# Kernel optimization log

Hardware: AMD Instinct MI355X
Metric: run time of the kernel (lower is better)

## Reference

```python
import jax, jax.numpy as jnp
import numpy as np

D_MODEL = 1024
N_HEADS = 16
HEAD_DIM = D_MODEL // N_HEADS
Q_PROJ = D_MODEL // 2
KV_PROJ = D_MODEL
INIT_SCALE = 0.02
EPS = 1e-5


def _ln(x, g, b):
    mu = jnp.mean(x, axis=-1, keepdims=True)
    var = jnp.mean(jnp.square(x - mu), axis=-1, keepdims=True)
    return (x - mu) * jax.lax.rsqrt(var + EPS) * g + b


def setup_inputs() -> dict:
    key = jax.random.key(0)
    ks = jax.random.split(key, 8)
    B, S = 2, 2048
    x = jax.random.normal(ks[0], (B, S, D_MODEL), dtype=jnp.float32)
    W_dq = INIT_SCALE * jax.random.normal(ks[1], (D_MODEL, Q_PROJ), dtype=jnp.float32)
    W_uq = INIT_SCALE * jax.random.normal(ks[2], (Q_PROJ, D_MODEL), dtype=jnp.float32)
    W_dkv = INIT_SCALE * jax.random.normal(ks[3], (D_MODEL, KV_PROJ), dtype=jnp.float32)
    W_ukv = INIT_SCALE * jax.random.normal(ks[4], (KV_PROJ, 2 * D_MODEL), dtype=jnp.float32)
    wo = INIT_SCALE * jax.random.normal(ks[5], (D_MODEL, D_MODEL), dtype=jnp.float32)
    return {
        "x": x,
        "W_dq": W_dq, "W_uq": W_uq,
        "q_ln_g": jnp.ones((Q_PROJ,), jnp.float32), "q_ln_b": jnp.zeros((Q_PROJ,), jnp.float32),
        "W_dkv": W_dkv, "W_ukv": W_ukv,
        "kv_ln_g": jnp.ones((KV_PROJ,), jnp.float32), "kv_ln_b": jnp.zeros((KV_PROJ,), jnp.float32),
        "preq_g": jnp.ones((D_MODEL,), jnp.float32), "preq_b": jnp.zeros((D_MODEL,), jnp.float32),
        "prekv_g": jnp.ones((D_MODEL,), jnp.float32), "prekv_b": jnp.zeros((D_MODEL,), jnp.float32),
        "wo": wo,
    }


def reference(x, W_dq, W_uq, q_ln_g, q_ln_b, W_dkv, W_ukv, kv_ln_g, kv_ln_b,
              preq_g, preq_b, prekv_g, prekv_b, wo):
    B, S, D = x.shape
    H, dh = N_HEADS, HEAD_DIM
    # Q path: pre-norm -> low-rank down -> LN -> up
    x_q = _ln(x, preq_g, preq_b)
    cq = _ln(x_q @ W_dq, q_ln_g, q_ln_b)            # [B,S,D/2]
    Q = (cq @ W_uq).reshape(B, S, H, dh)             # [B,S,H,dh]
    Q = Q / jnp.sqrt(jnp.asarray(dh, x.dtype))
    # KV path: pre-norm -> compress -> LN -> up, split into K,V
    x_kv = _ln(x, prekv_g, prekv_b)
    ckv = _ln(x_kv @ W_dkv, kv_ln_g, kv_ln_b)        # [B,S,D]
    KV = ckv @ W_ukv                                 # [B,S,2D]
    K, V = jnp.split(KV, 2, axis=-1)
    K = K.reshape(B, S, H, dh)
    V = V.reshape(B, S, H, dh)
    # causal attention (scores materialized as in original)
    scores = jnp.einsum('bqhd,bkhd->bhqk', Q, K)     # [B,H,S,S]
    causal = jnp.tril(jnp.ones((S, S), dtype=bool))  # True where allowed
    scores = jnp.where(causal[None, None], scores, jnp.asarray(-jnp.inf, scores.dtype))
    attn = jax.nn.softmax(scores, axis=-1)
    out = jnp.einsum('bhqk,bkhd->bqhd', attn, V).reshape(B, S, D)
    return out @ wo.T
```

## Files before the change

### kernel.cpp

```cpp
#include <hip/hip_runtime.h>
#include <hip/hip_bf16.h>

#define SEQ   2048
#define BATCH 2
#define NROWS 4096
#define DM    1024
#define NHEAD 16
#define DH    64
#define QP    512
#define KVP   1024
#define CH    8

typedef unsigned short us;
typedef ushort4 us4;
using bf16x8 = __attribute__((ext_vector_type(8))) __bf16;
using f32x4  = __attribute__((ext_vector_type(4))) float;

__device__ __forceinline__ us f2bf(float f) {
  union { __hip_bfloat16 h; us u; } cv;
  cv.h = __float2bfloat16(f);
  return cv.u;
}
__device__ __forceinline__ float bf2f(us u) {
  union { unsigned int u32; float f; } cv;
  cv.u32 = ((unsigned int)u) << 16;
  return cv.f;
}
__device__ __forceinline__ float loadp(const void* p, long i, int isbf) {
  return isbf ? bf2f(((const us*)p)[i]) : ((const float*)p)[i];
}
__device__ __forceinline__ void async16(const void* g, void* l) {
  __builtin_amdgcn_global_load_lds((__attribute__((address_space(1))) void*)g,
                                   (__attribute__((address_space(3))) void*)l,
                                   16, 0, 0);
}

__global__ void detect_dtype(const us* __restrict__ xu, int* __restrict__ flag) {
  __shared__ int red[256];
  const int tid = threadIdx.x;
  int cnt = 0;
  for (int i = tid; i < 4096; i += 256) {
    const int e = (xu[i] >> 7) & 0xff;
    if (e == 0 || (e >= 100 && e <= 134)) cnt++;
  }
  red[tid] = cnt;
  __syncthreads();
  for (int s = 128; s; s >>= 1) {
    if (tid < s) red[tid] += red[tid + s];
    __syncthreads();
  }
  if (tid == 0) *flag = (red[0] >= 3900) ? 1 : 0;
}

struct TD { const void* in; us* out; int R, C, nt, trans; };

__global__ __launch_bounds__(256) void stage0(
    TD t0, TD t1, TD t2, TD t3, TD t4,
    float4* __restrict__ zp, int n4,
    const void* __restrict__ xin,
    const void* __restrict__ g1, const void* __restrict__ b1,
    const void* __restrict__ g2, const void* __restrict__ b2,
    us* __restrict__ out1, us* __restrict__ out2,
    const int* __restrict__ flag)
{
  __shared__ us tile[32][33];
  __shared__ float red[8];
  __shared__ float musd[2];
  const int tid = threadIdx.x;
  const int isbf = *flag;
  int lin = blockIdx.x;

  if (lin < 5120) {
    TD t = t0;
    if (lin >= t.nt) { lin -= t.nt; t = t1;
      if (lin >= t.nt) { lin -= t.nt; t = t2;
        if (lin >= t.nt) { lin -= t.nt; t = t3;
          if (lin >= t.nt) { lin -= t.nt; t = t4; } } } }
    const int ntx = t.C >> 5;
    const int by = lin / ntx, bx = lin - by * ntx;
    const int tx = tid & 31, ty = tid >> 5;
    const long r0 = (long)by * 32, c0 = (long)bx * 32;
    if (t.trans) {
#pragma unroll
      for (int i = 0; i < 32; i += 8)
        tile[ty + i][tx] = isbf ? ((const us*)t.in)[(r0 + ty + i) * t.C + c0 + tx]
                                : f2bf(((const float*)t.in)[(r0 + ty + i) * t.C + c0 + tx]);
      __syncthreads();
#pragma unroll
      for (int i = 0; i < 32; i += 8)
        t.out[(c0 + ty + i) * t.R + r0 + tx] = tile[tx][ty + i];
    } else {
#pragma unroll
      for (int i = 0; i < 32; i += 8)
        t.out[(r0 + ty + i) * t.C + c0 + tx] =
            isbf ? ((const us*)t.in)[(r0 + ty + i) * t.C + c0 + tx]
                 : f2bf(((const float*)t.in)[(r0 + ty + i) * t.C + c0 + tx]);
    }
    return;
  }
  if (lin < 6144) {
    const float4 z = {0.f, 0.f, 0.f, 0.f};
    for (int i = (lin - 5120) * 256 + tid; i < n4; i += 1024 * 256) zp[i] = z;
    return;
  }
  const long row = lin - 6144;
  float v[4];
  float s = 0.f, s2 = 0.f;
#pragma unroll
  for (int i = 0; i < 4; i++) {
    const long c = tid + i * 256;
    const float t = loadp(xin, row * 1024 + c, isbf);
    v[i] = t; s += t; s2 += t * t;
  }
#pragma unroll
  for (int off = 32; off > 0; off >>= 1) {
    s  += __shfl_down(s,  off);
    s2 += __shfl_down(s2, off);
  }
  const int wave = tid >> 6, lane = tid & 63;
  if (lane == 0) { red[wave] = s; red[4 + wave] = s2; }
  __syncthreads();
  if (tid == 0) {
    const float ts = red[0] + red[1] + red[2] + red[3];
    const float t2 = red[4] + red[5] + red[6] + red[7];
    const float mu = ts * (1.f / 1024.f);
    const float var = t2 * (1.f / 1024.f) - mu * mu;
    musd[0] = mu; musd[1] = rsqrtf(var + 1e-5f);
  }
  __syncthreads();
  const float mu = musd[0], rs = musd[1];
#pragma unroll
  for (int i = 0; i < 4; i++) {
    const long c = tid + i * 256;
    const float nrm = (v[i] - mu) * rs;
    out1[row * 1024 + c] = f2bf(nrm * loadp(g1, c, isbf) + loadp(b1, c, isbf));
    out2[row * 1024 + c] = f2bf(nrm * loadp(g2, c, isbf) + loadp(b2, c, isbf));
  }
}

template<int C>
__device__ __forceinline__ void ln_body(const us* __restrict__ in,
                                        const void* __restrict__ g, const void* __restrict__ b,
                                        us* __restrict__ out, long row, int tid, int isbf) {
  constexpr int NP = C / 256;
  float v[NP];
  float s = 0.f, s2 = 0.f;
#pragma unroll
  for (int i = 0; i < NP; i++) {
    const float t = bf2f(in[row * C + tid + i * 256]);
    v[i] = t; s += t; s2 += t * t;
  }
#pragma unroll
  for (int off = 32; off > 0; off >>= 1) {
    s  += __shfl_down(s,  off);
    s2 += __shfl_down(s2, off);
  }
  __shared__ float red[8];
  __shared__ float musd[2];
  const int wave = tid >> 6, lane = tid & 63;
  if (lane == 0) { red[wave] = s; red[4 + wave] = s2; }
  __syncthreads();
  if (tid == 0) {
    const float ts = red[0] + red[1] + red[2] + red[3];
    const float t2 = red[4] + red[5] + red[6] + red[7];
    const float mu = ts * (1.f / C);
    const float var = t2 * (1.f / C) - mu * mu;
    musd[0] = mu; musd[1] = rsqrtf(var + 1e-5f);
  }
  __syncthreads();
  const float mu = musd[0], rs = musd[1];
#pragma unroll
  for (int i = 0; i < NP; i++) {
    const long c = tid + i * 256;
    out[row * C + c] = f2bf((v[i] - mu) * rs * loadp(g, c, isbf) + loadp(b, c, isbf));
  }
}

__global__ __launch_bounds__(256) void ln_rows_pair(
    const us* __restrict__ inq, const void* __restrict__ qg, const void* __restrict__ qb,
    us* __restrict__ outq,
    const us* __restrict__ inkv, const void* __restrict__ kvg, const void* __restrict__ kvb,
    us* __restrict__ outkv,
    const int* __restrict__ flag)
{
  const int isbf = *flag;
  if (blockIdx.x < NROWS)
    ln_body<512>(inq, qg, qb, outq, blockIdx.x, threadIdx.x, isbf);
  else
    ln_body<1024>(inkv, kvg, kvb, outkv, blockIdx.x - NROWS, threadIdx.x, isbf);
}

struct GD { const us* A; const us* Bt; void* C; int N, K, nxs; float scale; int omode; };

__global__ __launch_bounds__(256) void gemm_mt(GD g0, GD g1, int nb0,
                                               const int* __restrict__ flag) {
  __shared__ us As[2][128 * 32];
  __shared__ us Bs[2][128 * 32];
  GD g;
  int lin = blockIdx.x;
  if (lin < nb0) g = g0; else { g = g1; lin -= nb0; }
  const int by = lin >> g.nxs;
  const int bx = lin - (by << g.nxs);
  const int N = g.N, K = g.K;

  const int tid  = threadIdx.x;
  const int lane = tid & 63;
  const int wave = tid >> 6;
  const int n16  = lane & 15;
  const int quad = lane >> 4;
  const long m0 = (long)by * 128;
  const long n0 = (long)bx * 128;
  const int wm = (wave >> 1) * 64;
  const int wn = (wave & 1) * 64;

  const f32x4 zero = {0.f, 0.f, 0.f, 0.f};
  f32x4 acc[4][4];
#pragma unroll
  for (int i = 0; i < 4; i++)
#pragma unroll
    for (int j = 0; j < 4; j++) acc[i][j] = zero;

  const int srow = tid >> 2;
  const int scol = (tid & 3) * 8;
  const us* Ag0 = g.A  + (m0 + srow) * K + scol;
  const us* Ag1 = g.A  + (m0 + 64 + srow) * K + scol;
  const us* Bg0 = g.Bt + (n0 + srow) * K + scol;
  const us* Bg1 = g.Bt + (n0 + 64 + srow) * K + scol;
  const int lds_off = srow * 32 + scol;

  for (int k0 = 0; k0 < K; k0 += 64) {
#pragma unroll
    for (int s = 0; s < 2; s++) {
      const int ks = k0 + s * 32;
      async16(Ag0 + ks, As[s] + lds_off);
      async16(Ag1 + ks, As[s] + 2048 + lds_off);
      async16(Bg0 + ks, Bs[s] + lds_off);
      async16(Bg1 + ks, Bs[s] + 2048 + lds_off);
    }
    __syncthreads();
#pragma unroll
    for (int s = 0; s < 2; s++) {
      bf16x8 af[4], bfv[4];
#pragma unroll
      for (int i = 0; i < 4; i++)
        af[i] = *(const bf16x8*)(As[s] + (wm + i * 16 + n16) * 32 + quad * 8);
#pragma unroll
      for (int j = 0; j < 4; j++)
        bfv[j] = *(const bf16x8*)(Bs[s] + (wn + j * 16 + n16) * 32 + quad * 8);
#pragma unroll
      for (int i = 0; i < 4; i++)
#pragma unroll
        for (int j = 0; j < 4; j++)
          acc[i][j] = __builtin_amdgcn_mfma_f32_16x16x32_bf16(af[i], bfv[j], acc[i][j], 0, 0, 0);
    }
    __syncthreads();
  }

  const bool obf = (g.omode == 1) || (g.omode == 2 && *flag != 0);
  float* Cf = (float*)g.C;
  us* Cb = (us*)g.C;
#pragma unroll
  for (int i = 0; i < 4; i++) {
    const long row = m0 + wm + i * 16 + quad * 4;
#pragma unroll
    for (int j = 0; j < 4; j++) {
      const long col = n0 + wn + j * 16 + n16;
#pragma unroll
      for (int r = 0; r < 4; r++) {
        const float v = acc[i][j][r] * g.scale;
        if (obf) Cb[(row + r) * N + col] = f2bf(v);
        else     Cf[(row + r) * N + col] = v;
      }
    }
  }
}

__global__ __launch_bounds__(256) void flash_attn(
    const us* __restrict__ Q, const us* __restrict__ KV,
    float* __restrict__ Oacc, float* __restrict__ Lacc)
{
  __shared__ us Ks[64 * 72];
  __shared__ us Vt[64 * 72];
  __shared__ us Ps[4][16 * 72];

  int lin = blockIdx.x;
  int qt = 31, nc = 0;
  for (; qt >= 0; --qt) { nc = (qt >> 3) + 1; if (lin < nc) break; lin -= nc; }
  const int chunk = lin;
  const int kt0 = chunk * CH;
  const int kt1 = min(kt0 + CH, qt + 1);

  const int h   = blockIdx.y;
  const int bb  = blockIdx.z;
  const int tid = threadIdx.x;
  const int lane = tid & 63;
  const int wave = tid >> 6;
  const int n16 = lane & 15;
  const int quad = lane >> 4;
  const int qbase = qt * 64;
  const long rowQ0 = (long)bb * SEQ;

  bf16x8 aq[2];
  {
    const long gq = (rowQ0 + qbase + wave * 16 + n16) * DM + h * DH;
    aq[0] = *(const bf16x8*)(Q + gq + quad * 8);
    aq[1] = *(const bf16x8*)(Q + gq + 32 + quad * 8);
  }

  const f32x4 zero = {0.f, 0.f, 0.f, 0.f};
  f32x4 oacc[4];
#pragma unroll
  for (int d = 0; d < 4; d++) oacc[d] = zero;
  float rsum = 0.f;

  const int kk_key = tid >> 3;
  const int kk_d8  = (tid & 7) * 8;
  const int vd  = tid & 63;
  const int vkb = (tid >> 6) * 8;

  const us* kgb = KV + (rowQ0 + kk_key) * 2048 + h * DH + kk_d8;
  const us* vgb = KV + (rowQ0 + vkb) * 2048 + KVP + h * DH + vd;

  uint4 kpre0, kpre1;
  us vraw[16];
  auto loadKV = [&](int kt) {
    const us* kg = kgb + (long)kt * (64 * 2048);
    kpre0 = *(const uint4*)kg;
    kpre1 = *(const uint4*)(kg + 32 * 2048);
    const us* vg = vgb + (long)kt * (64 * 2048);
#pragma unroll
    for (int j = 0; j < 8; j++) vraw[j] = vg[j * 2048];
    const us* vg2 = vg + 32 * 2048;
#pragma unroll
    for (int j = 0; j < 8; j++) vraw[8 + j] = vg2[j * 2048];
  };
  loadKV(kt0);

  for (int kt = kt0; kt < kt1; kt++) {
    __syncthreads();
    *(uint4*)(Ks + kk_key * 72 + kk_d8)        = kpre0;
    *(uint4*)(Ks + (kk_key + 32) * 72 + kk_d8) = kpre1;
    {
      uint4 p0, p1;
      p0.x = (unsigned)vraw[0]  | ((unsigned)vraw[1]  << 16);
      p0.y = (unsigned)vraw[2]  | ((unsigned)vraw[3]  << 16);
      p0.z = (unsigned)vraw[4]  | ((unsigned)vraw[5]  << 16);
      p0.w = (unsigned)vraw[6]  | ((unsigned)vraw[7]  << 16);
      p1.x = (unsigned)vraw[8]  | ((unsigned)vraw[9]  << 16);
      p1.y = (unsigned)vraw[10] | ((unsigned)vraw[11] << 16);
      p1.z = (unsigned)vraw[12] | ((unsigned)vraw[13] << 16);
      p1.w = (unsigned)vraw[14] | ((unsigned)vraw[15] << 16);
      *(uint4*)(Vt + vd * 72 + vkb)      = p0;
      *(uint4*)(Vt + vd * 72 + vkb + 32) = p1;
    }
    __syncthreads();
    if (kt + 1 < kt1) loadKV(kt + 1);

    f32x4 sv[4];
#pragma unroll
    for (int j = 0; j < 4; j++) {
      const bf16x8 ak0 = *(const bf16x8*)(Ks + (j * 16 + n16) * 72 + quad * 8);
      const bf16x8 ak1 = *(const bf16x8*)(Ks + (j * 16 + n16) * 72 + 32 + quad * 8);
      f32x4 s = zero;
      s = __builtin_amdgcn_mfma_f32_16x16x32_bf16(ak0, aq[0], s, 0, 0, 0);
      s = __builtin_amdgcn_mfma_f32_16x16x32_bf16(ak1, aq[1], s, 0, 0, 0);
      sv[j] = s;
    }

    if (kt == qt) {
      const int qrl = wave * 16 + n16;
#pragma unroll
      for (int j = 0; j < 4; j++) {
        const int kl = j * 16 + quad * 4;
#pragma unroll
        for (int r = 0; r < 4; r++)
          sv[j][r] = (kl + r <= qrl) ? sv[j][r] : -1e30f;
      }
    }

    us* Pw = Ps[wave];
#pragma unroll
    for (int j = 0; j < 4; j++) {
      const float p0 = __builtin_amdgcn_exp2f(sv[j][0]);
      const float p1 = __builtin_amdgcn_exp2f(sv[j][1]);
      const float p2 = __builtin_amdgcn_exp2f(sv[j][2]);
      const float p3 = __builtin_amdgcn_exp2f(sv[j][3]);
      rsum += (p0 + p1) + (p2 + p3);
      us4 pk;
      pk.x = f2bf(p0); pk.y = f2bf(p1); pk.z = f2bf(p2); pk.w = f2bf(p3);
      *(us4*)(Pw + n16 * 72 + j * 16 + quad * 4) = pk;
    }
    __asm__ volatile("s_waitcnt lgkmcnt(0)" ::: "memory");

#pragma unroll
    for (int kc = 0; kc < 2; kc++) {
      const bf16x8 ap = *(const bf16x8*)(Pw + n16 * 72 + kc * 32 + quad * 8);
#pragma unroll
      for (int d = 0; d < 4; d++) {
        const bf16x8 bv = *(const bf16x8*)(Vt + (d * 16 + n16) * 72 + kc * 32 + quad * 8);
        oacc[d] = __builtin_amdgcn_mfma_f32_16x16x32_bf16(ap, bv, oacc[d], 0, 0, 0);
      }
    }
  }

  rsum += __shfl_xor(rsum, 16);
  rsum += __shfl_xor(rsum, 32);

  const long rw0 = rowQ0 + qbase + wave * 16;
  if (quad == 0)
    atomicAdd(&Lacc[(rw0 + n16) * NHEAD + h], rsum);
#pragma unroll
  for (int r = 0; r < 4; r++) {
    float* dst = Oacc + (rw0 + quad * 4 + r) * DM + h * DH + n16;
#pragma unroll
    for (int d = 0; d < 4; d++)
      atomicAdd(dst + d * 16, oacc[d][r]);
  }
}

__global__ __launch_bounds__(256) void flash_combine(
    const float* __restrict__ Oacc, const float* __restrict__ Lacc,
    us* __restrict__ O)
{
  __shared__ float invl[NHEAD];
  const long row = blockIdx.x;
  const int tid = threadIdx.x;
  if (tid < NHEAD) invl[tid] = 1.f / Lacc[row * NHEAD + tid];
  __syncthreads();
#pragma unroll
  for (int i = 0; i < 4; i++) {
    const int col = tid + i * 256;
    O[row * DM + col] = f2bf(Oacc[row * DM + col] * invl[col >> 6]);
  }
}

extern "C" void kernel_launch(void* const* d_in, const int* in_sizes, int n_in,
                              void* d_out, int out_size, void* d_ws, size_t ws_size,
                              hipStream_t stream) {
  const void* x      = d_in[0];
  const void* Wdq    = d_in[1];
  const void* Wuq    = d_in[2];
  const void* qg     = d_in[3];
  const void* qb     = d_in[4];
  const void* Wdkv   = d_in[5];
  const void* Wukv   = d_in[6];
  const void* kvg    = d_in[7];
  const void* kvb    = d_in[8];
  const void* preqg  = d_in[9];
  const void* preqb  = d_in[10];
  const void* prekvg = d_in[11];
  const void* prekvb = d_in[12];
  const void* wo     = d_in[13];

  char* ws = (char*)d_ws;
  const long MB = 1 << 20;
  int* flag   = (int*)ws;
  us* wdq_t   = (us*)(ws + 1 * MB);
  us* wuq_t   = (us*)(ws + 2 * MB);
  us* wdkv_t  = (us*)(ws + 3 * MB);
  us* wukv_t  = (us*)(ws + 5 * MB);
  us* wo_c    = (us*)(ws + 9 * MB);
  us* xq      = (us*)(ws + 11 * MB);
  us* xkv     = (us*)(ws + 19 * MB);
  float* Oacc = (float*)(ws + 27 * MB);
  float* Lacc = (float*)(ws + 43 * MB);
  us* obuf    = (us*)(ws + 43 * MB + 256 * 1024);
  us* tq_bf   = obuf;
  us* cq      = (us*)(ws + 43 * MB + 256 * 1024 + 8 * MB);
  us* qbuf    = (us*)(ws + 43 * MB + 256 * 1024 + 12 * MB);
  us* tkv_bf  = qbuf;
  us* ckv     = (us*)(ws + 43 * MB + 256 * 1024 + 20 * MB);
  us* kv      = (us*)(ws + 43 * MB + 256 * 1024 + 28 * MB);

  detect_dtype<<<1, 256, 0, stream>>>((const us*)x, flag);

  {
    TD t0 = { Wdq,  wdq_t,  1024,  512,  512, 1 };
    TD t1 = { Wuq,  wuq_t,   512, 1024,  512, 1 };
    TD t2 = { Wdkv, wdkv_t, 1024, 1024, 1024, 1 };
    TD t3 = { Wukv, wukv_t, 1024, 2048, 2048, 1 };
    TD t4 = { wo,   wo_c,   1024, 1024, 1024, 0 };
    const int n4 = (16 * 1024 * 1024 + 256 * 1024) / 16;
    stage0<<<10240, 256, 0, stream>>>(t0, t1, t2, t3, t4,
                                      (float4*)Oacc, n4,
                                      x, preqg, preqb, prekvg, prekvb, xq, xkv, flag);
  }

  {
    GD g0 = { xq,  wdq_t,  tq_bf,   512, 1024, 2, 1.f, 1 };
    GD g1 = { xkv, wdkv_t, tkv_bf, 1024, 1024, 3, 1.f, 1 };
    gemm_mt<<<384, 256, 0, stream>>>(g0, g1, 128, flag);
  }

  ln_rows_pair<<<2 * NROWS, 256, 0, stream>>>(tq_bf, qg, qb, cq, tkv_bf, kvg, kvb, ckv, flag);

  {
    GD g0 = { cq,  wuq_t,  qbuf, 1024,  512, 3, 0.125f * 1.44269504f, 1 };
    GD g1 = { ckv, wukv_t, kv,   2048, 1024, 4, 1.f, 1 };
    gemm_mt<<<768, 256, 0, stream>>>(g0, g1, 256, flag);
  }

  flash_attn<<<dim3(80, NHEAD, BATCH), 256, 0, stream>>>(qbuf, kv, Oacc, Lacc);
  flash_combine<<<NROWS, 256, 0, stream>>>(Oacc, Lacc, obuf);

  {
    GD g0 = { obuf, wo_c, d_out, 1024, 1024, 3, 1.f, 2 };
    gemm_mt<<<256, 256, 0, stream>>>(g0, g0, 256, flag);
  }
}
```

Baseline: 277.2 us.

## Keep softmax probabilities in registers by permuting V key layout for PV MFMA

Result: slower. 352.4 us (+27.1%).

```diff
diff --git a/kernel.cpp b/kernel.cpp
--- a/kernel.cpp
+++ b/kernel.cpp
@@ -275,13 +275,12 @@
   }
 }
 
-__global__ __launch_bounds__(256) void flash_attn(
+__global__ __launch_bounds__(256, 8) void flash_attn(
     const us* __restrict__ Q, const us* __restrict__ KV,
     float* __restrict__ Oacc, float* __restrict__ Lacc)
 {
   __shared__ us Ks[64 * 72];
   __shared__ us Vt[64 * 72];
-  __shared__ us Ps[4][16 * 72];
 
   int lin = blockIdx.x;
   int qt = 31, nc = 0;
@@ -316,10 +315,11 @@
   const int kk_key = tid >> 3;
   const int kk_d8  = (tid & 7) * 8;
   const int vd  = tid & 63;
-  const int vkb = (tid >> 6) * 8;
+  const int vw  = tid >> 6;
+  const int vkb = vw * 8;
 
   const us* kgb = KV + (rowQ0 + kk_key) * 2048 + h * DH + kk_d8;
-  const us* vgb = KV + (rowQ0 + vkb) * 2048 + KVP + h * DH + vd;
+  const us* vgb = KV + (rowQ0 + vw * 4) * 2048 + KVP + h * DH + vd;
 
   uint4 kpre0, kpre1;
   us vraw[16];
@@ -329,10 +329,12 @@
     kpre1 = *(const uint4*)(kg + 32 * 2048);
     const us* vg = vgb + (long)kt * (64 * 2048);
 #pragma unroll
-    for (int j = 0; j < 8; j++) vraw[j] = vg[j * 2048];
-    const us* vg2 = vg + 32 * 2048;
-#pragma unroll
-    for (int j = 0; j < 8; j++) vraw[8 + j] = vg2[j * 2048];
+    for (int r = 0; r < 4; r++) {
+      vraw[r]      = vg[r * 2048];
+      vraw[4 + r]  = vg[(16 + r) * 2048];
+      vraw[8 + r]  = vg[(32 + r) * 2048];
+      vraw[12 + r] = vg[(48 + r) * 2048];
+    }
   };
   loadKV(kt0);
 
@@ -378,7 +380,7 @@
       }
     }
 
-    us* Pw = Ps[wave];
+    unsigned pep[4][2];
 #pragma unroll
     for (int j = 0; j < 4; j++) {
       const float p0 = __builtin_amdgcn_exp2f(sv[j][0]);
@@ -386,21 +388,25 @@
       const float p2 = __builtin_amdgcn_exp2f(sv[j][2]);
       const float p3 = __builtin_amdgcn_exp2f(sv[j][3]);
       rsum += (p0 + p1) + (p2 + p3);
-      us4 pk;
-      pk.x = f2bf(p0); pk.y = f2bf(p1); pk.z = f2bf(p2); pk.w = f2bf(p3);
-      *(us4*)(Pw + n16 * 72 + j * 16 + quad * 4) = pk;
-    }
-    __asm__ volatile("s_waitcnt lgkmcnt(0)" ::: "memory");
-
+      pep[j][0] = (unsigned)f2bf(p0) | ((unsigned)f2bf(p1) << 16);
+      pep[j][1] = (unsigned)f2bf(p2) | ((unsigned)f2bf(p3) << 16);
+    }
+
+    __builtin_amdgcn_s_setprio(1);
 #pragma unroll
     for (int kc = 0; kc < 2; kc++) {
-      const bf16x8 ap = *(const bf16x8*)(Pw + n16 * 72 + kc * 32 + quad * 8);
+      union { bf16x8 v; unsigned u[4]; } apu;
+      apu.u[0] = pep[2 * kc][0];
+      apu.u[1] = pep[2 * kc][1];
+      apu.u[2] = pep[2 * kc + 1][0];
+      apu.u[3] = pep[2 * kc + 1][1];
 #pragma unroll
       for (int d = 0; d < 4; d++) {
         const bf16x8 bv = *(const bf16x8*)(Vt + (d * 16 + n16) * 72 + kc * 32 + quad * 8);
-        oacc[d] = __builtin_amdgcn_mfma_f32_16x16x32_bf16(ap, bv, oacc[d], 0, 0, 0);
+        oacc[d] = __builtin_amdgcn_mfma_f32_16x16x32_bf16(apu.v, bv, oacc[d], 0, 0, 0);
       }
     }
+    __builtin_amdgcn_s_setprio(0);
   }
 
   rsum += __shfl_xor(rsum, 16);
```
